# Optimization experiments

Hardware: AMD Instinct MI355X
Metric: run time of the kernel (lower is better)

Reference implementation:

```python
import jax, jax.numpy as jnp
import numpy as np

IN_Q, OUT_Q = 32, 32
GRID_H, GRID_W = 64, 64
FREQ_H, FREQ_W = GRID_H, GRID_W // 2 + 1
BATCH = 32
INIT_SCALE = 0.02


def setup_inputs() -> dict:
    key = jax.random.key(0)
    keys = jax.random.split(key, 9)
    inp = {"x": jax.random.normal(keys[0], (BATCH, 4 * IN_Q, GRID_H, GRID_W), dtype=jnp.float32)}
    names = ["kr_w", "kr_x", "kr_y", "kr_z", "ki_w", "ki_x", "ki_y", "ki_z"]
    for i, n in enumerate(names):
        inp[n] = jax.random.normal(keys[i + 1], (IN_Q, OUT_Q, FREQ_H, FREQ_W), dtype=jnp.float32) * INIT_SCALE
    return inp


def reference(x, kr_w, kr_x, kr_y, kr_z, ki_w, ki_x, ki_y, ki_z):
    q = IN_Q
    # Split quaternion components and FFT each: [B, q, H, Wf] complex
    xs = jnp.stack([x[:, :q], x[:, q:2 * q], x[:, 2 * q:3 * q], x[:, 3 * q:]])  # [4,B,q,H,W]
    Xs = jnp.fft.rfft2(xs, s=(GRID_H, GRID_W), axes=(-2, -1))  # [4,B,q,H,Wf]
    # Complex kernels, stacked: [4, in_q, out_q, H, Wf]
    Ws = jnp.stack([kr_w + 1j * ki_w, kr_x + 1j * ki_x, kr_y + 1j * ki_y, kr_z + 1j * ki_z])
    # All 16 pairwise contractions in one einsum: C[p,q] = W_p contracted with X_q
    C = jnp.einsum('piohw,qbihw->pqbohw', Ws, Xs)  # [4,4,B,out,H,Wf]
    # Hamilton product combination
    Pw = C[0, 0] - C[1, 1] - C[2, 2] - C[3, 3]
    Px = C[0, 1] + C[1, 0] + C[2, 3] - C[3, 2]
    Py = C[0, 2] - C[1, 3] + C[2, 0] + C[3, 1]
    Pz = C[0, 3] + C[1, 2] - C[2, 1] + C[3, 0]
    P = jnp.stack([Pw, Px, Py, Pz])  # [4,B,out,H,Wf]
    o = jnp.fft.irfft2(P, s=(GRID_H, GRID_W), axes=(-2, -1))  # [4,B,out,H,W]
    # cat along channel dim: [B, 4*out, H, W]
    return jnp.concatenate([o[0], o[1], o[2], o[3]], axis=1)
```

## Files before the change

### kernel.cpp

```cpp
#include <hip/hip_runtime.h>

#define FH 64
#define FW 64
#define NWF 33
#define NBIN (FH*NWF)
#define NIMG 4096
#define PI2 6.283185307179586f

typedef unsigned short u16;
typedef unsigned int u32;
typedef __attribute__((ext_vector_type(8))) short bf16x8;
typedef __attribute__((ext_vector_type(8))) _Float16 f16x8;
typedef __attribute__((ext_vector_type(4))) unsigned short u16x4;
typedef __attribute__((ext_vector_type(4))) float f32x4;
typedef __attribute__((ext_vector_type(4))) int   i32x4;

__device__ __forceinline__ u16 f2bf(float f) {
    unsigned u = __float_as_uint(f);
    unsigned r = (u + 0x7FFFu + ((u >> 16) & 1u)) >> 16;
    return (u16)r;
}
__device__ __forceinline__ u16 f2h(float f) {
    _Float16 h = (_Float16)f;
    return __builtin_bit_cast(u16, h);
}
__device__ __forceinline__ float2 upk(u32 v) {
    return make_float2(__uint_as_float(v << 16), __uint_as_float(v & 0xFFFF0000u));
}
__device__ __forceinline__ u32 pk(float2 v) {
    return (u32)f2bf(v.x) | ((u32)f2bf(v.y) << 16);
}
__device__ __forceinline__ f16x8 negh(f16x8 v) {
    i32x4 t = __builtin_bit_cast(i32x4, v);
    t ^= (int)0x80008000;
    return __builtin_bit_cast(f16x8, t);
}

__global__ __launch_bounds__(512, 4) void fwd_prep_kernel(
    const float* __restrict__ x, u32* __restrict__ Xs,
    const float* __restrict__ s0, const float* __restrict__ s1,
    const float* __restrict__ s2, const float* __restrict__ s3,
    const float* __restrict__ s4, const float* __restrict__ s5,
    const float* __restrict__ s6, const float* __restrict__ s7,
    u16* __restrict__ WT)
{
    __shared__ __align__(16) u16 sm[36096];
    const int tid  = threadIdx.x;
    const int lane = tid & 63;
    const int wid  = tid >> 6;
    const int a16  = lane & 15;
    const int kg   = lane >> 4;

    u16* mats0 = sm;
    u16* mats1 = sm + 4608;
    u16* sre   = sm + 9216 + wid*2304;
    u16* sim   = sre + 1152;
    u16* lds2  = sm + 27648;

    for (int t = tid; t < 4096; t += 512) {
        int a = t >> 6, bb = t & 63;
        float sn, cs;
        __sincosf(PI2 * (float)((a*bb) & 63) * (1.f/64.f), &sn, &cs);
        mats0[a*72 + bb] = f2h(cs);
        mats1[a*72 + bb] = f2h(sn);
    }
    __syncthreads();

    for (int item = blockIdx.x; item < 2624; item += 512) {
        const int grp = item / 41;
        const int rem = item - grp*41;
        if (rem < 8) {
            const int img = (grp*8 + rem)*8 + wid;
            const int qc = img >> 10;
            const int b  = (img >> 5) & 31;
            const int ci = img & 31;
            const float* __restrict__ src = x + ((size_t)b*128 + (size_t)qc*32 + ci) * (FH*FW);

            f16x8 xf[4][2];
            #pragma unroll
            for (int mt = 0; mt < 4; ++mt)
                #pragma unroll
                for (int ks = 0; ks < 2; ++ks) {
                    const float* rp = src + (16*mt + a16)*64 + ks*32 + kg*8;
                    float4 v0 = *(const float4*)rp;
                    float4 v1 = *(const float4*)(rp + 4);
                    xf[mt][ks] = (f16x8){ (_Float16)v0.x, (_Float16)v0.y, (_Float16)v0.z, (_Float16)v0.w,
                                          (_Float16)v1.x, (_Float16)v1.y, (_Float16)v1.z, (_Float16)v1.w };
                }

            u32* __restrict__ dst = Xs + (size_t)img * NBIN;
            #pragma unroll
            for (int nt = 0; nt < 3; ++nt) {
                f32x4 are[4], aim[4];
                #pragma unroll
                for (int mt = 0; mt < 4; ++mt) { are[mt] = (f32x4){0,0,0,0}; aim[mt] = (f32x4){0,0,0,0}; }
                #pragma unroll
                for (int ks = 0; ks < 2; ++ks) {
                    const int rb = (16*nt + a16)*72 + ks*32 + kg*8;
                    f16x8 cf  = *(const f16x8*)&mats0[rb];
                    f16x8 nsf = negh(*(const f16x8*)&mats1[rb]);
                    #pragma unroll
                    for (int mt = 0; mt < 4; ++mt) {
                        are[mt] = __builtin_amdgcn_mfma_f32_16x16x32_f16(xf[mt][ks], cf,  are[mt], 0, 0, 0);
                        aim[mt] = __builtin_amdgcn_mfma_f32_16x16x32_f16(xf[mt][ks], nsf, aim[mt], 0, 0, 0);
                    }
                }
                #pragma unroll
                for (int mt = 0; mt < 4; ++mt) {
                    u16x4 re4 = { f2h(are[mt][0]), f2h(are[mt][1]), f2h(are[mt][2]), f2h(are[mt][3]) };
                    u16x4 im4 = { f2h(aim[mt][0]), f2h(aim[mt][1]), f2h(aim[mt][2]), f2h(aim[mt][3]) };
                    *(u16x4*)&sre[a16*72 + 16*mt + 4*kg] = re4;
                    *(u16x4*)&sim[a16*72 + 16*mt + 4*kg] = im4;
                }
                f16x8 br[2], bi[2];
                #pragma unroll
                for (int ks = 0; ks < 2; ++ks) {
                    br[ks] = *(const f16x8*)&sre[a16*72 + ks*32 + kg*8];
                    bi[ks] = *(const f16x8*)&sim[a16*72 + ks*32 + kg*8];
                }
                const int k = 16*nt + a16;
                #pragma unroll
                for (int mt2 = 0; mt2 < 4; ++mt2) {
                    f32x4 xre = (f32x4){0,0,0,0}, xim = (f32x4){0,0,0,0};
                    #pragma unroll
                    for (int ks = 0; ks < 2; ++ks) {
                        const int rb = (16*mt2 + a16)*72 + ks*32 + kg*8;
                        f16x8 cf = *(const f16x8*)&mats0[rb];
                        f16x8 sf = *(const f16x8*)&mats1[rb];
                        xre = __builtin_amdgcn_mfma_f32_16x16x32_f16(cf, br[ks], xre, 0, 0, 0);
                        xre = __builtin_amdgcn_mfma_f32_16x16x32_f16(sf, bi[ks], xre, 0, 0, 0);
                        xim = __builtin_amdgcn_mfma_f32_16x16x32_f16(cf, bi[ks], xim, 0, 0, 0);
                        xim = __builtin_amdgcn_mfma_f32_16x16x32_f16(negh(sf), br[ks], xim, 0, 0, 0);
                    }
                    if (k < 33) {
                        #pragma unroll
                        for (int r = 0; r < 4; ++r)
                            dst[(16*mt2 + 4*kg + r)*33 + k] = pk(make_float2(xre[r], xim[r]));
                    }
                }
            }
        } else {
            const int pb = grp*33 + (rem - 8);
            const int bt = pb % 66;
            const int ay = pb / 66;
            const int a  = ay >> 2;
            const int o0 = (ay & 3) * 8;
            const float* __restrict__ src =
                (a==0)?s0:(a==1)?s1:(a==2)?s2:(a==3)?s3:(a==4)?s4:(a==5)?s5:(a==6)?s6:s7;
            const int bin0 = bt * 32;

            #pragma unroll
            for (int it = 0; it < 4; ++it) {
                int e = tid + it*512;
                int f4 = e & 7, rt = e >> 3;
                int i = rt & 31, oo = rt >> 5;
                int io = i*32 + o0 + oo;
                float4 v = ((const float4*)src)[(size_t)io*(NBIN/4) + bt*8 + f4];
                int chL = oo*32 + i;
                int bb = f4*4;
                lds2[(bb+0)*264 + chL] = f2bf(v.x);
                lds2[(bb+1)*264 + chL] = f2bf(v.y);
                lds2[(bb+2)*264 + chL] = f2bf(v.z);
                lds2[(bb+3)*264 + chL] = f2bf(v.w);
            }
            __syncthreads();
            const int p = a & 3, ri = a >> 2;
            #pragma unroll
            for (int it = 0; it < 2; ++it) {
                int e = tid + it*512;
                int binL = e >> 5, c8 = e & 31;
                bf16x8 v = *(const bf16x8*)&lds2[binL*264 + c8*8];
                size_t d = ((size_t)(bin0 + binL)*8 + p*2 + ri)*1024 + o0*32 + c8*8;
                *(bf16x8*)(WT + d) = v;
            }
            __syncthreads();
        }
    }
}

__global__ __launch_bounds__(256) void xpose_x_kernel(const u32* __restrict__ Xs,
                                                      u32* __restrict__ XT)
{
    const int g    = blockIdx.x;
    const int bin0 = blockIdx.y * 32;
    __shared__ u32 tile[32][33];
    const int tid = threadIdx.x;
    #pragma unroll
    for (int it = 0; it < 4; ++it) {
        int e = tid + it*256;
        int imgL = e >> 5, binL = e & 31;
        tile[imgL][binL] = Xs[(size_t)(g*32 + imgL) * NBIN + bin0 + binL];
    }
    __syncthreads();
    const int q = g >> 5, b = g & 31;
    #pragma unroll
    for (int it = 0; it < 2; ++it) {
        int e = tid + it*256;
        int binL = e >> 4, pr = e & 15;
        u32 v0 = tile[pr*2][binL], v1 = tile[pr*2 + 1][binL];
        u32 re = (v0 & 0xFFFFu) | (v1 << 16);
        u32 im = (v0 >> 16) | (v1 & 0xFFFF0000u);
        size_t base = ((size_t)(bin0 + binL)*8 + q*2) * 512 + b*16 + pr;
        XT[base]       = re;
        XT[base + 512] = im;
    }
}

__global__ __launch_bounds__(256) void contract_kernel(
    const u16* __restrict__ XT, const u16* __restrict__ WT,
    u32* __restrict__ P)
{
    const int bid  = blockIdx.x;
    const int bin  = (bid & 7) * (NBIN/8) + (bid >> 3);
    const int wid  = threadIdx.x >> 6;
    const int lane = threadIdx.x & 63;
    const int bh = wid >> 1, oh = wid & 1;
    const int row = lane & 15, kg = lane >> 4;

    const u16* __restrict__ xb = XT + (size_t)bin * 8192;
    const u16* __restrict__ wb = WT + (size_t)bin * 8192;

    bf16x8 ax[4][2];
    #pragma unroll
    for (int q = 0; q < 4; ++q)
        #pragma unroll
        for (int ri = 0; ri < 2; ++ri)
            ax[q][ri] = *(const bf16x8*)(xb + ((q*2 + ri)*32 + bh*16 + row)*32 + kg*8);

    bf16x8 wpos[4][2], wneg[4][2];
    #pragma unroll
    for (int p = 0; p < 4; ++p)
        #pragma unroll
        for (int ri = 0; ri < 2; ++ri) {
            bf16x8 w = *(const bf16x8*)(wb + ((p*2 + ri)*32 + oh*16 + row)*32 + kg*8);
            wpos[p][ri] = w;
            i32x4 t = __builtin_bit_cast(i32x4, w);
            t ^= (int)0x80008000;
            wneg[p][ri] = __builtin_bit_cast(bf16x8, t);
        }

    f32x4 acc[4][2];
    #pragma unroll
    for (int c = 0; c < 4; ++c)
        #pragma unroll
        for (int ri = 0; ri < 2; ++ri)
            acc[c][ri] = (f32x4){0.f, 0.f, 0.f, 0.f};

    constexpr int PI_[4][4] = {{0,1,2,3},{1,0,3,2},{2,3,0,1},{3,2,1,0}};
    constexpr int SG_[4][4] = {{1,-1,-1,-1},{1,1,-1,1},{1,1,1,-1},{1,-1,1,1}};
    #pragma unroll
    for (int c = 0; c < 4; ++c)
        #pragma unroll
        for (int q = 0; q < 4; ++q) {
            const int  p   = PI_[c][q];
            const bool pos = SG_[c][q] > 0;
            bf16x8 wr_s = pos ? wpos[p][0] : wneg[p][0];
            bf16x8 wi_s = pos ? wpos[p][1] : wneg[p][1];
            bf16x8 wi_m = pos ? wneg[p][1] : wpos[p][1];
            acc[c][0] = __builtin_amdgcn_mfma_f32_16x16x32_bf16(ax[q][0], wr_s, acc[c][0], 0, 0, 0);
            acc[c][0] = __builtin_amdgcn_mfma_f32_16x16x32_bf16(ax[q][1], wi_m, acc[c][0], 0, 0, 0);
            acc[c][1] = __builtin_amdgcn_mfma_f32_16x16x32_bf16(ax[q][1], wr_s, acc[c][1], 0, 0, 0);
            acc[c][1] = __builtin_amdgcn_mfma_f32_16x16x32_bf16(ax[q][0], wi_s, acc[c][1], 0, 0, 0);
        }

    u32* __restrict__ dst = P + (size_t)bin * 4096;
    #pragma unroll
    for (int c = 0; c < 4; ++c)
        #pragma unroll
        for (int r = 0; r < 4; ++r) {
            int b_ = bh*16 + kg*4 + r;
            int o  = oh*16 + row;
            dst[c*1024 + b_*32 + o] = pk(make_float2(acc[c][0][r], acc[c][1][r]));
        }
}

__global__ __launch_bounds__(512, 4) void fft_inv_kernel(const u32* __restrict__ P,
                                                         float* __restrict__ out)
{
    __shared__ __align__(16) u16 mats[2][64*72];
    __shared__ __align__(16) u16 wbuf[4][7168];

    const int tid  = threadIdx.x;
    const int lane = tid & 63;
    const int wid  = tid >> 6;
    const int slot = wid >> 1;
    const int half = wid & 1;
    const int ltid = (half << 6) | lane;
    const int a16  = lane & 15;
    const int q    = lane >> 4;

    const int bid = blockIdx.x;
    const int g   = (bid & 7) * 128 + (bid >> 3);
    const int img = g * 4 + slot;
    const int c  = img >> 10;
    const int b  = (img >> 5) & 31;
    const int oc = img & 31;

    for (int t = tid; t < 4096; t += 512) {
        int a = t >> 6, bb = t & 63;
        float sn, cs;
        __sincosf(PI2 * (float)((a*bb) & 63) * (1.f/64.f), &sn, &cs);
        mats[0][a*72 + bb] = f2h(cs);
        mats[1][a*72 + bb] = f2h(sn);
    }

    {
        u16* ETre = wbuf[slot];
        u16* ETim = wbuf[slot] + 48*72;
        for (int j = 33*72 + ltid; j < 48*72; j += 128) {
            ETre[j] = 0;
            ETim[j] = 0;
        }
    }
    for (int e = tid; e < NBIN*4; e += 512) {
        int bin = e >> 2, sl = e & 3;
        u32 v = P[(size_t)bin * 4096 + g*4 + sl];
        float2 f = upk(v);
        int hf = bin / 33, k = bin - hf*33;
        u16* ETre = wbuf[sl];
        u16* ETim = wbuf[sl] + 48*72;
        ETre[k*72 + hf] = f2h(f.x);
        ETim[k*72 + hf] = f2h(f.y);
    }
    __syncthreads();

    u16* ETre = wbuf[slot];
    u16* ETim = wbuf[slot] + 48*72;
    f16x8 ere[2][2], eim[2][2];
    #pragma unroll
    for (int mtl = 0; mtl < 2; ++mtl) {
        const int mt = 2*half + mtl;
        if (mt < 3) {
            #pragma unroll
            for (int ks = 0; ks < 2; ++ks) {
                ere[mtl][ks] = *(const f16x8*)&ETre[(16*mt + a16)*72 + ks*32 + q*8];
                eim[mtl][ks] = *(const f16x8*)&ETim[(16*mt + a16)*72 + ks*32 + q*8];
            }
        }
    }
    __syncthreads();

    u16* Tre = wbuf[slot];
    u16* Tim = wbuf[slot] + 64*56;
    #pragma unroll
    for (int mtl = 0; mtl < 2; ++mtl) {
        const int mt = 2*half + mtl;
        if (mt < 3) {
            #pragma unroll
            for (int nt = 0; nt < 4; ++nt) {
                f32x4 tre = (f32x4){0,0,0,0}, tim = (f32x4){0,0,0,0};
                #pragma unroll
                for (int ks = 0; ks < 2; ++ks) {
                    const int rb = (16*nt + a16)*72 + ks*32 + q*8;
                    f16x8 cf = *(const f16x8*)&mats[0][rb];
                    f16x8 sf = *(const f16x8*)&mats[1][rb];
                    tre = __builtin_amdgcn_mfma_f32_16x16x32_f16(ere[mtl][ks], cf, tre, 0, 0, 0);
                    tre = __builtin_amdgcn_mfma_f32_16x16x32_f16(eim[mtl][ks], negh(sf), tre, 0, 0, 0);
                    tim = __builtin_amdgcn_mfma_f32_16x16x32_f16(ere[mtl][ks], sf, tim, 0, 0, 0);
                    tim = __builtin_amdgcn_mfma_f32_16x16x32_f16(eim[mtl][ks], cf, tim, 0, 0, 0);
                }
                const int m0 = 16*mt + 4*q;
                u16x4 r4, i4;
                #pragma unroll
                for (int r = 0; r < 4; ++r) {
                    int m = m0 + r;
                    float s = (m == 0 || m == 32) ? (1.f/4096.f) : (2.f/4096.f);
                    r4[r] = (m < 33) ? f2h(tre[r] * s) : (u16)0;
                    i4[r] = (m < 33) ? f2h(tim[r] * s) : (u16)0;
                }
                *(u16x4*)&Tre[(16*nt + a16)*56 + m0] = r4;
                *(u16x4*)&Tim[(16*nt + a16)*56 + m0] = i4;
            }
        }
    }
    __syncthreads();

    float* __restrict__ dst = out + ((size_t)b*128 + (size_t)c*32 + oc) * (FH*FW);
    #pragma unroll
    for (int mtl = 0; mtl < 2; ++mtl) {
        const int mt = 2*half + mtl;
        f16x8 tfr[2], tfi[2];
        #pragma unroll
        for (int ks = 0; ks < 2; ++ks) {
            const int mbase = ks*32 + q*8;
            if (mbase < 48) {
                tfr[ks] = *(const f16x8*)&Tre[(16*mt + a16)*56 + mbase];
                tfi[ks] = *(const f16x8*)&Tim[(16*mt + a16)*56 + mbase];
            } else {
                tfr[ks] = (f16x8){0,0,0,0,0,0,0,0};
                tfi[ks] = (f16x8){0,0,0,0,0,0,0,0};
            }
        }
        #pragma unroll
        for (int nt = 0; nt < 4; ++nt) {
            f32x4 acc = (f32x4){0,0,0,0};
            #pragma unroll
            for (int ks = 0; ks < 2; ++ks) {
                const int rb = (16*nt + a16)*72 + ks*32 + q*8;
                f16x8 cf = *(const f16x8*)&mats[0][rb];
                f16x8 sf = *(const f16x8*)&mats[1][rb];
                acc = __builtin_amdgcn_mfma_f32_16x16x32_f16(tfr[ks], cf, acc, 0, 0, 0);
                acc = __builtin_amdgcn_mfma_f32_16x16x32_f16(tfi[ks], negh(sf), acc, 0, 0, 0);
            }
            #pragma unroll
            for (int r = 0; r < 4; ++r)
                dst[(16*mt + 4*q + r)*64 + 16*nt + a16] = acc[r];
        }
    }
}

extern "C" void kernel_launch(void* const* d_in, const int* in_sizes, int n_in,
                              void* d_out, int out_size, void* d_ws, size_t ws_size,
                              hipStream_t stream)
{
    const float* x   = (const float*)d_in[0];
    const float* krw = (const float*)d_in[1];
    const float* krx = (const float*)d_in[2];
    const float* kry = (const float*)d_in[3];
    const float* krz = (const float*)d_in[4];
    const float* kiw = (const float*)d_in[5];
    const float* kix = (const float*)d_in[6];
    const float* kiy = (const float*)d_in[7];
    const float* kiz = (const float*)d_in[8];

    const size_t R = (size_t)NBIN * 8192 * sizeof(u16);
    u16* XT = (u16*)d_ws;
    u16* WT = (u16*)((char*)d_ws + R);
    u32* Xs = (u32*)((char*)d_ws + 2*R);
    u32* P  = Xs;
    float* out = (float*)d_out;

    fwd_prep_kernel<<<dim3(512), 512, 0, stream>>>(x, Xs,
                                                   krw, krx, kry, krz,
                                                   kiw, kix, kiy, kiz, WT);
    xpose_x_kernel<<<dim3(128, NBIN/32), 256, 0, stream>>>(Xs, (u32*)XT);
    contract_kernel<<<dim3(NBIN), 256, 0, stream>>>(XT, WT, P);
    fft_inv_kernel<<<dim3(NIMG/4), 512, 0, stream>>>(P, out);
}
```

Baseline: 124.8 us.

## Launch one block per work item and transpose FFT intermediates via lane shuffles

The forward prep kernel switches from a 512-block grid-stride loop to a 2624-block grid with one item per block. This cuts shared memory from about 72KB to 18KB and lets weight-transpose blocks skip building the twiddle tables entirely. The row-FFT intermediate is now repacked to fp16 and moved between lanes with __shfl instead of a round trip through per-wave LDS buffers. In exchange, the FFT blocks now rebuild the sincos tables for every item instead of once per block, and the shuffles add cross-lane traffic.

```diff
diff --git a/kernel.cpp b/kernel.cpp
--- a/kernel.cpp
+++ b/kernel.cpp
@@ -12,6 +12,7 @@
 typedef __attribute__((ext_vector_type(8))) short bf16x8;
 typedef __attribute__((ext_vector_type(8))) _Float16 f16x8;
 typedef __attribute__((ext_vector_type(4))) unsigned short u16x4;
+typedef __attribute__((ext_vector_type(4))) unsigned int u32x4;
 typedef __attribute__((ext_vector_type(4))) float f32x4;
 typedef __attribute__((ext_vector_type(4))) int   i32x4;
 
@@ -23,6 +24,9 @@
 __device__ __forceinline__ u16 f2h(float f) {
     _Float16 h = (_Float16)f;
     return __builtin_bit_cast(u16, h);
+}
+__device__ __forceinline__ u32 pkh(float a, float b) {
+    return (u32)f2h(a) | ((u32)f2h(b) << 16);
 }
 __device__ __forceinline__ float2 upk(u32 v) {
     return make_float2(__uint_as_float(v << 16), __uint_as_float(v & 0xFFFF0000u));
@@ -44,136 +48,145 @@
     const float* __restrict__ s6, const float* __restrict__ s7,
     u16* __restrict__ WT)
 {
-    __shared__ __align__(16) u16 sm[36096];
-    const int tid  = threadIdx.x;
-    const int lane = tid & 63;
-    const int wid  = tid >> 6;
-    const int a16  = lane & 15;
-    const int kg   = lane >> 4;
-
-    u16* mats0 = sm;
-    u16* mats1 = sm + 4608;
-    u16* sre   = sm + 9216 + wid*2304;
-    u16* sim   = sre + 1152;
-    u16* lds2  = sm + 27648;
-
-    for (int t = tid; t < 4096; t += 512) {
-        int a = t >> 6, bb = t & 63;
-        float sn, cs;
-        __sincosf(PI2 * (float)((a*bb) & 63) * (1.f/64.f), &sn, &cs);
-        mats0[a*72 + bb] = f2h(cs);
-        mats1[a*72 + bb] = f2h(sn);
-    }
-    __syncthreads();
-
-    for (int item = blockIdx.x; item < 2624; item += 512) {
-        const int grp = item / 41;
-        const int rem = item - grp*41;
-        if (rem < 8) {
-            const int img = (grp*8 + rem)*8 + wid;
-            const int qc = img >> 10;
-            const int b  = (img >> 5) & 31;
-            const int ci = img & 31;
-            const float* __restrict__ src = x + ((size_t)b*128 + (size_t)qc*32 + ci) * (FH*FW);
-
-            f16x8 xf[4][2];
-            #pragma unroll
-            for (int mt = 0; mt < 4; ++mt)
+    __shared__ __align__(16) u16 sm[9216];
+    const int tid = threadIdx.x;
+    const int grp = blockIdx.x / 41;
+    const int rem = blockIdx.x - grp*41;
+
+    if (rem < 8) {
+        const int lane = tid & 63;
+        const int wid  = tid >> 6;
+        const int a16  = lane & 15;
+        const int kg   = lane >> 4;
+
+        u16* mats0 = sm;
+        u16* mats1 = sm + 4608;
+
+        for (int t = tid; t < 4096; t += 512) {
+            int a = t >> 6, bb = t & 63;
+            float sn, cs;
+            __sincosf(PI2 * (float)((a*bb) & 63) * (1.f/64.f), &sn, &cs);
+            mats0[a*72 + bb] = f2h(cs);
+            mats1[a*72 + bb] = f2h(sn);
+        }
+        __syncthreads();
+
+        const int img = (grp*8 + rem)*8 + wid;
+        const int qc = img >> 10;
+        const int b  = (img >> 5) & 31;
+        const int ci = img & 31;
+        const float* __restrict__ src = x + ((size_t)b*128 + (size_t)qc*32 + ci) * (FH*FW);
+
+        f16x8 xf[4][2];
+        #pragma unroll
+        for (int mt = 0; mt < 4; ++mt)
+            #pragma unroll
+            for (int ks = 0; ks < 2; ++ks) {
+                const float* rp = src + (16*mt + a16)*64 + ks*32 + kg*8;
+                float4 v0 = *(const float4*)rp;
+                float4 v1 = *(const float4*)(rp + 4);
+                xf[mt][ks] = (f16x8){ (_Float16)v0.x, (_Float16)v0.y, (_Float16)v0.z, (_Float16)v0.w,
+                                      (_Float16)v1.x, (_Float16)v1.y, (_Float16)v1.z, (_Float16)v1.w };
+            }
+
+        u32* __restrict__ dst = Xs + (size_t)img * NBIN;
+
+        #pragma unroll
+        for (int nt = 0; nt < 3; ++nt) {
+            f32x4 are[4], aim[4];
+            #pragma unroll
+            for (int mt = 0; mt < 4; ++mt) { are[mt] = (f32x4){0,0,0,0}; aim[mt] = (f32x4){0,0,0,0}; }
+            #pragma unroll
+            for (int ks = 0; ks < 2; ++ks) {
+                const int rb = (16*nt + a16)*72 + ks*32 + kg*8;
+                f16x8 cf  = *(const f16x8*)&mats0[rb];
+                f16x8 nsf = negh(*(const f16x8*)&mats1[rb]);
+                #pragma unroll
+                for (int mt = 0; mt < 4; ++mt) {
+                    are[mt] = __builtin_amdgcn_mfma_f32_16x16x32_f16(xf[mt][ks], cf,  are[mt], 0, 0, 0);
+                    aim[mt] = __builtin_amdgcn_mfma_f32_16x16x32_f16(xf[mt][ks], nsf, aim[mt], 0, 0, 0);
+                }
+            }
+            u32 pre[4][2], pim[4][2];
+            #pragma unroll
+            for (int mt = 0; mt < 4; ++mt) {
+                pre[mt][0] = pkh(are[mt][0], are[mt][1]);
+                pre[mt][1] = pkh(are[mt][2], are[mt][3]);
+                pim[mt][0] = pkh(aim[mt][0], aim[mt][1]);
+                pim[mt][1] = pkh(aim[mt][2], aim[mt][3]);
+            }
+            f16x8 br[2], bi[2];
+            #pragma unroll
+            for (int ks = 0; ks < 2; ++ks) {
+                u32 brw[4], biw[4];
+                #pragma unroll
+                for (int w = 0; w < 4; ++w) {
+                    const int srcl = a16 + 16*((2*kg + (w >> 1)) & 3);
+                    u32 tA = __shfl(pre[2*ks][w & 1],     srcl, 64);
+                    u32 tB = __shfl(pre[2*ks + 1][w & 1], srcl, 64);
+                    brw[w] = (kg < 2) ? tA : tB;
+                    u32 uA = __shfl(pim[2*ks][w & 1],     srcl, 64);
+                    u32 uB = __shfl(pim[2*ks + 1][w & 1], srcl, 64);
+                    biw[w] = (kg < 2) ? uA : uB;
+                }
+                br[ks] = __builtin_bit_cast(f16x8, (u32x4){brw[0], brw[1], brw[2], brw[3]});
+                bi[ks] = __builtin_bit_cast(f16x8, (u32x4){biw[0], biw[1], biw[2], biw[3]});
+            }
+            const int k = 16*nt + a16;
+            #pragma unroll
+            for (int mt2 = 0; mt2 < 4; ++mt2) {
+                f32x4 xre = (f32x4){0,0,0,0}, xim = (f32x4){0,0,0,0};
                 #pragma unroll
                 for (int ks = 0; ks < 2; ++ks) {
-                    const float* rp = src + (16*mt + a16)*64 + ks*32 + kg*8;
-                    float4 v0 = *(const float4*)rp;
-                    float4 v1 = *(const float4*)(rp + 4);
-                    xf[mt][ks] = (f16x8){ (_Float16)v0.x, (_Float16)v0.y, (_Float16)v0.z, (_Float16)v0.w,
-                                          (_Float16)v1.x, (_Float16)v1.y, (_Float16)v1.z, (_Float16)v1.w };
-                }
-
-            u32* __restrict__ dst = Xs + (size_t)img * NBIN;
-            #pragma unroll
-            for (int nt = 0; nt < 3; ++nt) {
-                f32x4 are[4], aim[4];
-                #pragma unroll
-                for (int mt = 0; mt < 4; ++mt) { are[mt] = (f32x4){0,0,0,0}; aim[mt] = (f32x4){0,0,0,0}; }
-                #pragma unroll
-                for (int ks = 0; ks < 2; ++ks) {
-                    const int rb = (16*nt + a16)*72 + ks*32 + kg*8;
-                    f16x8 cf  = *(const f16x8*)&mats0[rb];
-                    f16x8 nsf = negh(*(const f16x8*)&mats1[rb]);
+                    const int rb = (16*mt2 + a16)*72 + ks*32 + kg*8;
+                    f16x8 cf = *(const f16x8*)&mats0[rb];
+                    f16x8 sf = *(const f16x8*)&mats1[rb];
+                    xre = __builtin_amdgcn_mfma_f32_16x16x32_f16(cf, br[ks], xre, 0, 0, 0);
+                    xre = __builtin_amdgcn_mfma_f32_16x16x32_f16(sf, bi[ks], xre, 0, 0, 0);
+                    xim = __builtin_amdgcn_mfma_f32_16x16x32_f16(cf, bi[ks], xim, 0, 0, 0);
+                    xim = __builtin_amdgcn_mfma_f32_16x16x32_f16(negh(sf), br[ks], xim, 0, 0, 0);
+                }
+                if (k < 33) {
                     #pragma unroll
-                    for (int mt = 0; mt < 4; ++mt) {
-                        are[mt] = __builtin_amdgcn_mfma_f32_16x16x32_f16(xf[mt][ks], cf,  are[mt], 0, 0, 0);
-                        aim[mt] = __builtin_amdgcn_mfma_f32_16x16x32_f16(xf[mt][ks], nsf, aim[mt], 0, 0, 0);
-                    }
-                }
-                #pragma unroll
-                for (int mt = 0; mt < 4; ++mt) {
-                    u16x4 re4 = { f2h(are[mt][0]), f2h(are[mt][1]), f2h(are[mt][2]), f2h(are[mt][3]) };
-                    u16x4 im4 = { f2h(aim[mt][0]), f2h(aim[mt][1]), f2h(aim[mt][2]), f2h(aim[mt][3]) };
-                    *(u16x4*)&sre[a16*72 + 16*mt + 4*kg] = re4;
-                    *(u16x4*)&sim[a16*72 + 16*mt + 4*kg] = im4;
-                }
-                f16x8 br[2], bi[2];
-                #pragma unroll
-                for (int ks = 0; ks < 2; ++ks) {
-                    br[ks] = *(const f16x8*)&sre[a16*72 + ks*32 + kg*8];
-                    bi[ks] = *(const f16x8*)&sim[a16*72 + ks*32 + kg*8];
-                }
-                const int k = 16*nt + a16;
-                #pragma unroll
-                for (int mt2 = 0; mt2 < 4; ++mt2) {
-                    f32x4 xre = (f32x4){0,0,0,0}, xim = (f32x4){0,0,0,0};
-                    #pragma unroll
-                    for (int ks = 0; ks < 2; ++ks) {
-                        const int rb = (16*mt2 + a16)*72 + ks*32 + kg*8;
-                        f16x8 cf = *(const f16x8*)&mats0[rb];
-                        f16x8 sf = *(const f16x8*)&mats1[rb];
-                        xre = __builtin_amdgcn_mfma_f32_16x16x32_f16(cf, br[ks], xre, 0, 0, 0);
-                        xre = __builtin_amdgcn_mfma_f32_16x16x32_f16(sf, bi[ks], xre, 0, 0, 0);
-                        xim = __builtin_amdgcn_mfma_f32_16x16x32_f16(cf, bi[ks], xim, 0, 0, 0);
-                        xim = __builtin_amdgcn_mfma_f32_16x16x32_f16(negh(sf), br[ks], xim, 0, 0, 0);
-                    }
-                    if (k < 33) {
-                        #pragma unroll
-                        for (int r = 0; r < 4; ++r)
-                            dst[(16*mt2 + 4*kg + r)*33 + k] = pk(make_float2(xre[r], xim[r]));
-                    }
-                }
-            }
-        } else {
-            const int pb = grp*33 + (rem - 8);
-            const int bt = pb % 66;
-            const int ay = pb / 66;
-            const int a  = ay >> 2;
-            const int o0 = (ay & 3) * 8;
-            const float* __restrict__ src =
-                (a==0)?s0:(a==1)?s1:(a==2)?s2:(a==3)?s3:(a==4)?s4:(a==5)?s5:(a==6)?s6:s7;
-            const int bin0 = bt * 32;
-
-            #pragma unroll
-            for (int it = 0; it < 4; ++it) {
-                int e = tid + it*512;
-                int f4 = e & 7, rt = e >> 3;
-                int i = rt & 31, oo = rt >> 5;
-                int io = i*32 + o0 + oo;
-                float4 v = ((const float4*)src)[(size_t)io*(NBIN/4) + bt*8 + f4];
-                int chL = oo*32 + i;
-                int bb = f4*4;
-                lds2[(bb+0)*264 + chL] = f2bf(v.x);
-                lds2[(bb+1)*264 + chL] = f2bf(v.y);
-                lds2[(bb+2)*264 + chL] = f2bf(v.z);
-                lds2[(bb+3)*264 + chL] = f2bf(v.w);
-            }
-            __syncthreads();
-            const int p = a & 3, ri = a >> 2;
-            #pragma unroll
-            for (int it = 0; it < 2; ++it) {
-                int e = tid + it*512;
-                int binL = e >> 5, c8 = e & 31;
-                bf16x8 v = *(const bf16x8*)&lds2[binL*264 + c8*8];
-                size_t d = ((size_t)(bin0 + binL)*8 + p*2 + ri)*1024 + o0*32 + c8*8;
-                *(bf16x8*)(WT + d) = v;
-            }
-            __syncthreads();
+                    for (int r = 0; r < 4; ++r)
+                        dst[(16*mt2 + 4*kg + r)*33 + k] = pk(make_float2(xre[r], xim[r]));
+                }
+            }
+        }
+    } else {
+        const int pb = grp*33 + (rem - 8);
+        const int bt = pb % 66;
+        const int ay = pb / 66;
+        const int a  = ay >> 2;
+        const int o0 = (ay & 3) * 8;
+        const float* __restrict__ src =
+            (a==0)?s0:(a==1)?s1:(a==2)?s2:(a==3)?s3:(a==4)?s4:(a==5)?s5:(a==6)?s6:s7;
+        const int bin0 = bt * 32;
+        u16* lds2 = sm;
+
+        #pragma unroll
+        for (int it = 0; it < 4; ++it) {
+            int e = tid + it*512;
+            int f4 = e & 7, rt = e >> 3;
+            int i = rt & 31, oo = rt >> 5;
+            int io = i*32 + o0 + oo;
+            float4 v = ((const float4*)src)[(size_t)io*(NBIN/4) + bt*8 + f4];
+            int chL = oo*32 + i;
+            int bb = f4*4;
+            lds2[(bb+0)*264 + chL] = f2bf(v.x);
+            lds2[(bb+1)*264 + chL] = f2bf(v.y);
+            lds2[(bb+2)*264 + chL] = f2bf(v.z);
+            lds2[(bb+3)*264 + chL] = f2bf(v.w);
+        }
+        __syncthreads();
+        const int p = a & 3, ri = a >> 2;
+        #pragma unroll
+        for (int it = 0; it < 2; ++it) {
+            int e = tid + it*512;
+            int binL = e >> 5, c8 = e & 31;
+            bf16x8 v = *(const bf16x8*)&lds2[binL*264 + c8*8];
+            size_t d = ((size_t)(bin0 + binL)*8 + p*2 + ri)*1024 + o0*32 + c8*8;
+            *(bf16x8*)(WT + d) = v;
         }
     }
 }
@@ -430,9 +443,9 @@
     u32* P  = Xs;
     float* out = (float*)d_out;
 
-    fwd_prep_kernel<<<dim3(512), 512, 0, stream>>>(x, Xs,
-                                                   krw, krx, kry, krz,
-                                                   kiw, kix, kiy, kiz, WT);
+    fwd_prep_kernel<<<dim3(2624), 512, 0, stream>>>(x, Xs,
+                                                    krw, krx, kry, krz,
+                                                    kiw, kix, kiy, kiz, WT);
     xpose_x_kernel<<<dim3(128, NBIN/32), 256, 0, stream>>>(Xs, (u32*)XT);
     contract_kernel<<<dim3(NBIN), 256, 0, stream>>>(XT, WT, P);
     fft_inv_kernel<<<dim3(NIMG/4), 512, 0, stream>>>(P, out);
```

Result: faster. 113.3 us (-9.2%).
